# Kernel optimization log

Hardware: AMD Instinct MI355X
Metric: run time of the kernel (lower is better)

The kernel has to match this reference:

```python
import jax, jax.numpy as jnp
import numpy as np
from jax import lax

PATCH = 17
THRESH = 0.5


def _bbox_from_mask(mask_np):
    # mask_np: [D,H,W] bool. Matches mask_to_3d_bbox (min/max of nonzero coords).
    z, y, x = np.nonzero(mask_np)
    return (int(x.min()), int(y.min()), int(z.min()),
            int(x.max()), int(y.max()), int(z.max()))


def _extract_patches(vol, bbox):
    # vol: [1,1,D,H,W]; crop uses exclusive max (slice z_min:z_max) like the torch code
    x0, y0, z0, x1, y1, z1 = bbox
    t = vol[:, :, z0:z1, y0:y1, x0:x1]
    pads = []
    for d in t.shape[2:]:
        r = d % PATCH
        p = (PATCH - r) % PATCH
        pads.append((p // 2, p - p // 2))
    t = jnp.pad(t, ((0, 0), (0, 0), pads[0], pads[1], pads[2]))
    D, H, W = t.shape[2:]
    nD, nH, nW = D // PATCH, H // PATCH, W // PATCH
    p = t.reshape(nD, PATCH, nH, PATCH, nW, PATCH)
    p = p.transpose(0, 2, 4, 1, 3, 5).reshape(-1, PATCH, PATCH, PATCH)
    return p[:, None]  # [N,1,17,17,17]


def _conv3d(x, w, b, stride):
    y = lax.conv_general_dilated(x, w, (stride,) * 3, 'VALID',
                                 dimension_numbers=('NCDHW', 'OIDHW', 'NCDHW'))
    return y + b.reshape(1, -1, 1, 1, 1)


def _model(fixed, moving, c1w, c1b, c2w, c2b, f1w, f1b, f2w, f2b):
    # Stand-in for the opaque torch.jit model: siamese-concat 3D CNN -> MLP -> tanh.
    x = jnp.concatenate([fixed, moving], axis=1)          # [N,2,17,17,17]
    x = jax.nn.relu(_conv3d(x, c1w, c1b, 2))              # [N,32,8,8,8]
    x = jax.nn.relu(_conv3d(x, c2w, c2b, 2))              # [N,64,3,3,3]
    x = x.reshape(x.shape[0], -1)                         # [N,1728]
    x = jax.nn.relu(x @ f1w.T + f1b)                      # [N,256]
    return jnp.tanh(x @ f2w.T + f2b)                      # [N,1]


def setup_inputs() -> dict:
    key = jax.random.key(0)
    ks = jax.random.split(key, 10)
    V = 222
    source = jax.random.normal(ks[0], (1, 1, V, V, V), jnp.float32)
    target = jax.random.uniform(ks[1], (1, 1, V, V, V), jnp.float32)
    fc_in = 64 * 3 * 3 * 3
    return {
        'source': source,
        'target': target,
        'conv1_w': jax.random.normal(ks[2], (32, 2, 3, 3, 3), jnp.float32) * 0.1,
        'conv1_b': jnp.zeros((32,), jnp.float32),
        'conv2_w': jax.random.normal(ks[3], (64, 32, 3, 3, 3), jnp.float32) * 0.05,
        'conv2_b': jnp.zeros((64,), jnp.float32),
        'fc1_w': jax.random.normal(ks[4], (256, fc_in), jnp.float32) * 0.02,
        'fc1_b': jnp.zeros((256,), jnp.float32),
        'fc2_w': jax.random.normal(ks[5], (1, 256), jnp.float32) * 0.05,
        'fc2_b': jnp.zeros((1,), jnp.float32),
    }


def reference(source, target, conv1_w, conv1_b, conv2_w, conv2_b,
              fc1_w, fc1_b, fc2_w, fc2_b):
    mask_np = np.asarray(target) > 0
    bbox = _bbox_from_mask(mask_np.squeeze())
    fixed_patches = _extract_patches(target, bbox)   # [N,1,17,17,17]
    moving_patches = _extract_patches(source, bbox)
    # per-patch zero fraction on fixed patches; keep if <= threshold
    zero_frac = jnp.mean((fixed_patches[:, 0] == 0).astype(jnp.float32), axis=(1, 2, 3))
    keep = (zero_frac <= THRESH).astype(jnp.float32)  # [N]
    out = _model(fixed_patches, moving_patches, conv1_w, conv1_b, conv2_w, conv2_b,
                 fc1_w, fc1_b, fc2_w, fc2_b)          # [N,1]
    # mean over kept patches == weighted mean (stream-compaction-free, same math)
    return jnp.sum(out[:, 0] * keep) / jnp.sum(keep)
```

## Files before the change

kernel.cpp:

```cpp
#include <hip/hip_runtime.h>


static constexpr int kPS = 433;
static constexpr int kRS = 25;
static constexpr int kCS = 528;
static constexpr int kZS = 66;
static constexpr int kHOff = 6912;

template <bool PACKED>
static __device__ __forceinline__ float2 dmr16_patch(
    int p, int t,
    const float* __restrict__ src, const float* __restrict__ tgt,
    const float* __restrict__ c1w, const float* __restrict__ c1b,
    const float* __restrict__ c2w, const float* __restrict__ c2b,
    const float* __restrict__ fw,  const float* __restrict__ f1b,
    const float* __restrict__ f2w, const float* __restrict__ f2b,
    float* __restrict__ sBuf, float* __restrict__ sRed) {
  int pd = p / 169; int rem = p - pd * 169; int phh = rem / 13; int pww = rem - phh * 13;
  int z0 = pd * 17, y0 = phh * 17, x0 = pww * 17;

  int wv  = t >> 6;
  int od  = (t >> 3) & 7, oh = t & 7;
  int oc2 = t & 63;

  float cnt = 0.f;
  for (int idx = t; idx < 4913; idx += 256) {
    int a = idx / 289; int r2 = idx - a * 289; int b = r2 / 17; int c = r2 - b * 17;
    float v = tgt[((size_t)(z0 + a) * 222 + (y0 + b)) * 222 + (x0 + c)];
    sBuf[a * kPS + b * kRS + c] = v;
    if (v == 0.0f) cnt += 1.f;
  }
  sRed[t] = cnt;
  __syncthreads();
  for (int o = 128; o > 0; o >>= 1) {
    if (t < o) sRed[t] += sRed[t + o];
    __syncthreads();
  }
  float keep = (sRed[0] / 4913.0f <= 0.5f) ? 1.0f : 0.0f;
  __syncthreads();

  float acc2[27];
  #pragma unroll
  for (int i = 0; i < 27; i++) acc2[i] = 0.f;

  #pragma unroll 1
  for (int half = 0; half < 2; half++) {
    float acc[4][8];
    #pragma unroll
    for (int i = 0; i < 4; i++)
      #pragma unroll
      for (int j = 0; j < 8; j++) acc[i][j] = 0.f;

    #pragma unroll 1
    for (int ic = 0; ic < 2; ic++) {
      if (half + ic > 0) {
        const float* vol = ic ? src : tgt;
        __syncthreads();
        for (int idx = t; idx < 4913; idx += 256) {
          int a = idx / 289; int r2 = idx - a * 289; int b = r2 / 17; int c = r2 - b * 17;
          sBuf[a * kPS + b * kRS + c] =
              vol[((size_t)(z0 + a) * 222 + (y0 + b)) * 222 + (x0 + c)];
        }
        __syncthreads();
      }
      #pragma unroll 1
      for (int td = 0; td < 3; td++) {
        #pragma unroll 1
        for (int th = 0; th < 3; th++) {
          int rbase = (2 * od + td) * kPS + (2 * oh + th) * kRS;
          float a[17];
          #pragma unroll
          for (int x = 0; x < 17; x++) a[x] = sBuf[rbase + x];
          #pragma unroll
          for (int ocr = 0; ocr < 4; ocr++) {
            int oc = half * 16 + wv * 4 + ocr;
            const float* wp = c1w + oc * 54 + ic * 27 + td * 9 + th * 3;
            float w0 = wp[0], w1 = wp[1], w2 = wp[2];
            #pragma unroll
            for (int ow = 0; ow < 8; ow++)
              acc[ocr][ow] += a[2 * ow] * w0 + a[2 * ow + 1] * w1 + a[2 * ow + 2] * w2;
          }
        }
      }
    }
    __syncthreads();
    #pragma unroll
    for (int ocr = 0; ocr < 4; ocr++) {
      int lo = wv * 4 + ocr;
      float b = c1b[half * 16 + lo];
      int base = lo * kCS + od * kZS + oh * 8;
      #pragma unroll
      for (int ow = 0; ow < 8; ow++)
        sBuf[base + ow] = fmaxf(acc[ocr][ow] + b, 0.f);
    }
    __syncthreads();

    #pragma unroll 1
    for (int icr = 0; icr < 4; icr++) {
      int icl = wv * 4 + icr;
      int ic  = half * 16 + icl;
      const float* cbase = sBuf + icl * kCS;
      #pragma unroll 1
      for (int td = 0; td < 3; td++) {
        #pragma unroll 1
        for (int th = 0; th < 3; th++) {
          const float* wp = c2w + oc2 * 864 + ic * 27 + td * 9 + th * 3;
          float w0 = wp[0], w1 = wp[1], w2 = wp[2];
          #pragma unroll
          for (int zo = 0; zo < 3; zo++) {
            #pragma unroll
            for (int yo = 0; yo < 3; yo++) {
              const float* rp = cbase + (2 * zo + td) * kZS + (2 * yo + th) * 8;
              #pragma unroll
              for (int xo = 0; xo < 3; xo++)
                acc2[zo * 9 + yo * 3 + xo] +=
                    rp[2 * xo] * w0 + rp[2 * xo + 1] * w1 + rp[2 * xo + 2] * w2;
            }
          }
        }
      }
    }
  }
  __syncthreads();
  #pragma unroll
  for (int pos = 0; pos < 27; pos++)
    sBuf[(wv * 27 + pos) * 64 + oc2] = acc2[pos];
  __syncthreads();
  float* sH = sBuf + kHOff;
  for (int idx = t; idx < 1728; idx += 256) {
    int o = idx & 63, pos = idx >> 6;
    float v = sBuf[pos * 64 + o] + sBuf[(27 + pos) * 64 + o] +
              sBuf[(54 + pos) * 64 + o] + sBuf[(81 + pos) * 64 + o];
    sH[o * 27 + pos] = fmaxf(v + c2b[o], 0.f);
  }
  __syncthreads();

  float acc1 = 0.f;
  if (PACKED) {
    const float4* w4p = (const float4*)fw;
    const float4* sH4 = (const float4*)sH;
    #pragma unroll 8
    for (int k4 = 0; k4 < 432; k4++) {
      float4 w  = w4p[k4 * 256 + t];
      float4 hv = sH4[k4];
      acc1 += w.x * hv.x + w.y * hv.y + w.z * hv.z + w.w * hv.w;
    }
  } else {
    const float* frow = fw + (size_t)t * 1728;
    #pragma unroll 8
    for (int k = 0; k < 1728; k++) acc1 += sH[k] * frow[k];
  }
  float h = fmaxf(acc1 + f1b[t], 0.f);
  sRed[t] = h * f2w[t];
  __syncthreads();
  for (int o = 128; o > 0; o >>= 1) {
    if (t < o) sRed[t] += sRed[t + o];
    __syncthreads();
  }
  float2 rk;
  rk.x = tanhf(sRed[0] + f2b[0]) * keep;
  rk.y = keep;
  __syncthreads();
  return rk;
}

__global__ void dmr16_tr(const float* __restrict__ f1w, float* __restrict__ w1t4) {
  int k4 = blockIdx.x;
  int n  = threadIdx.x;
  const float* s = f1w + (size_t)n * 1728 + k4 * 4;
  float4 w;
  w.x = s[0]; w.y = s[1]; w.z = s[2]; w.w = s[3];
  ((float4*)w1t4)[k4 * 256 + n] = w;
}

__global__ __launch_bounds__(256, 4)
void DMMRLoss_52621939310662_kernel(
    const float* __restrict__ src, const float* __restrict__ tgt,
    const float* __restrict__ c1w, const float* __restrict__ c1b,
    const float* __restrict__ c2w, const float* __restrict__ c2b,
    const float* __restrict__ w1t4, const float* __restrict__ f1b,
    const float* __restrict__ f2w, const float* __restrict__ f2b,
    float* __restrict__ pr, float* __restrict__ pk) {
  __shared__ float sBuf[8704];
  __shared__ float sRed[256];
  int t = threadIdx.x;
  float2 rk = dmr16_patch<true>(blockIdx.x, t, src, tgt, c1w, c1b, c2w, c2b,
                                w1t4, f1b, f2w, f2b, sBuf, sRed);
  if (t == 0) { pr[blockIdx.x] = rk.x; pk[blockIdx.x] = rk.y; }
}

__global__ __launch_bounds__(256, 4)
void dmr16_hot_raw(const float* __restrict__ src, const float* __restrict__ tgt,
                   const float* __restrict__ c1w, const float* __restrict__ c1b,
                   const float* __restrict__ c2w, const float* __restrict__ c2b,
                   const float* __restrict__ f1w, const float* __restrict__ f1b,
                   const float* __restrict__ f2w, const float* __restrict__ f2b,
                   float* __restrict__ pr, float* __restrict__ pk) {
  __shared__ float sBuf[8704];
  __shared__ float sRed[256];
  int t = threadIdx.x;
  float2 rk = dmr16_patch<false>(blockIdx.x, t, src, tgt, c1w, c1b, c2w, c2b,
                                 f1w, f1b, f2w, f2b, sBuf, sRed);
  if (t == 0) { pr[blockIdx.x] = rk.x; pk[blockIdx.x] = rk.y; }
}

__global__ void dmr16_reduce(const float* __restrict__ pr, const float* __restrict__ pk,
                             float* __restrict__ out) {
  __shared__ float s1[256], s2[256];
  int t = threadIdx.x;
  float a = 0.f, b = 0.f;
  for (int p = t; p < 2197; p += 256) { a += pr[p]; b += pk[p]; }
  s1[t] = a; s2[t] = b;
  __syncthreads();
  for (int o = 128; o > 0; o >>= 1) {
    if (t < o) { s1[t] += s1[t + o]; s2[t] += s2[t + o]; }
    __syncthreads();
  }
  if (t == 0) out[0] = s1[0] / s2[0];
}

__global__ __launch_bounds__(256, 4)
void dmr16_solo(const float* __restrict__ src, const float* __restrict__ tgt,
                const float* __restrict__ c1w, const float* __restrict__ c1b,
                const float* __restrict__ c2w, const float* __restrict__ c2b,
                const float* __restrict__ f1w, const float* __restrict__ f1b,
                const float* __restrict__ f2w, const float* __restrict__ f2b,
                float* __restrict__ out) {
  __shared__ float sBuf[8704];
  __shared__ float sRed[256];
  __shared__ float sAcc[2];
  int t = threadIdx.x;
  if (t == 0) { sAcc[0] = 0.f; sAcc[1] = 0.f; }
  for (int p = 0; p < 2197; p++) {
    __syncthreads();
    float2 rk = dmr16_patch<false>(p, t, src, tgt, c1w, c1b, c2w, c2b,
                                   f1w, f1b, f2w, f2b, sBuf, sRed);
    if (t == 0) { sAcc[0] += rk.x; sAcc[1] += rk.y; }
  }
  __syncthreads();
  if (t == 0) out[0] = sAcc[0] / sAcc[1];
}

extern "C" void kernel_launch(void* const* d_in, const int* in_sizes, int n_in,
                              void* d_out, int out_size, void* d_ws, size_t ws_size,
                              hipStream_t stream) {
  const float* src = (const float*)d_in[0];
  const float* tgt = (const float*)d_in[1];
  const float* c1w = (const float*)d_in[2];
  const float* c1b = (const float*)d_in[3];
  const float* c2w = (const float*)d_in[4];
  const float* c2b = (const float*)d_in[5];
  const float* f1w = (const float*)d_in[6];
  const float* f1b = (const float*)d_in[7];
  const float* f2w = (const float*)d_in[8];
  const float* f2b = (const float*)d_in[9];
  float* out = (float*)d_out;

  const size_t nW1T = 442368;
  const size_t nPK  = 2 * 2197;
  if (d_ws && ws_size >= (nW1T + nPK) * sizeof(float)) {
    float* w1t4 = (float*)d_ws;
    float* pr   = w1t4 + nW1T;
    float* pk   = pr + 2197;
    dmr16_tr<<<432, 256, 0, stream>>>(f1w, w1t4);
    DMMRLoss_52621939310662_kernel<<<2197, 256, 0, stream>>>(
        src, tgt, c1w, c1b, c2w, c2b, w1t4, f1b, f2w, f2b, pr, pk);
    dmr16_reduce<<<1, 256, 0, stream>>>(pr, pk, out);
  } else if (d_ws && ws_size >= nPK * sizeof(float)) {
    float* pr = (float*)d_ws;
    float* pk = pr + 2197;
    dmr16_hot_raw<<<2197, 256, 0, stream>>>(
        src, tgt, c1w, c1b, c2w, c2b, f1w, f1b, f2w, f2b, pr, pk);
    dmr16_reduce<<<1, 256, 0, stream>>>(pr, pk, out);
  } else {
    dmr16_solo<<<1, 256, 0, stream>>>(
        src, tgt, c1w, c1b, c2w, c2b, f1w, f1b, f2w, f2b, out);
  }
}
```

Before: 437.8 us.

## Repack conv2 weights as float4, vectorize conv1 output stores and conv2 LDS reads

```diff
diff --git a/kernel.cpp b/kernel.cpp
--- a/kernel.cpp
+++ b/kernel.cpp
@@ -3,23 +3,24 @@
 
 static constexpr int kPS = 433;
 static constexpr int kRS = 25;
-static constexpr int kCS = 528;
-static constexpr int kZS = 66;
+static constexpr int kCS = 552;
+static constexpr int kZS = 68;
 static constexpr int kHOff = 6912;
 
-template <bool PACKED>
-static __device__ __forceinline__ float2 dmr16_patch(
+template <bool WPACK>
+static __device__ __forceinline__ float2 dmr17_patch(
     int p, int t,
     const float* __restrict__ src, const float* __restrict__ tgt,
     const float* __restrict__ c1w, const float* __restrict__ c1b,
     const float* __restrict__ c2w, const float* __restrict__ c2b,
-    const float* __restrict__ fw,  const float* __restrict__ f1b,
+    const float* __restrict__ w2t4,
+    const float* __restrict__ fw1, const float* __restrict__ f1b,
     const float* __restrict__ f2w, const float* __restrict__ f2b,
     float* __restrict__ sBuf, float* __restrict__ sRed) {
   int pd = p / 169; int rem = p - pd * 169; int phh = rem / 13; int pww = rem - phh * 13;
   int z0 = pd * 17, y0 = phh * 17, x0 = pww * 17;
 
-  int wv  = t >> 6;
+  int wvu = __builtin_amdgcn_readfirstlane(t >> 6);
   int od  = (t >> 3) & 7, oh = t & 7;
   int oc2 = t & 63;
 
@@ -73,7 +74,7 @@
           for (int x = 0; x < 17; x++) a[x] = sBuf[rbase + x];
           #pragma unroll
           for (int ocr = 0; ocr < 4; ocr++) {
-            int oc = half * 16 + wv * 4 + ocr;
+            int oc = half * 16 + wvu * 4 + ocr;
             const float* wp = c1w + oc * 54 + ic * 27 + td * 9 + th * 3;
             float w0 = wp[0], w1 = wp[1], w2 = wp[2];
             #pragma unroll
@@ -86,35 +87,46 @@
     __syncthreads();
     #pragma unroll
     for (int ocr = 0; ocr < 4; ocr++) {
-      int lo = wv * 4 + ocr;
+      int lo = wvu * 4 + ocr;
       float b = c1b[half * 16 + lo];
       int base = lo * kCS + od * kZS + oh * 8;
-      #pragma unroll
-      for (int ow = 0; ow < 8; ow++)
-        sBuf[base + ow] = fmaxf(acc[ocr][ow] + b, 0.f);
+      float4 v0, v1;
+      v0.x = fmaxf(acc[ocr][0] + b, 0.f); v0.y = fmaxf(acc[ocr][1] + b, 0.f);
+      v0.z = fmaxf(acc[ocr][2] + b, 0.f); v0.w = fmaxf(acc[ocr][3] + b, 0.f);
+      v1.x = fmaxf(acc[ocr][4] + b, 0.f); v1.y = fmaxf(acc[ocr][5] + b, 0.f);
+      v1.z = fmaxf(acc[ocr][6] + b, 0.f); v1.w = fmaxf(acc[ocr][7] + b, 0.f);
+      *(float4*)&sBuf[base]     = v0;
+      *(float4*)&sBuf[base + 4] = v1;
     }
     __syncthreads();
 
     #pragma unroll 1
     for (int icr = 0; icr < 4; icr++) {
-      int icl = wv * 4 + icr;
+      int icl = wvu * 4 + icr;
       int ic  = half * 16 + icl;
       const float* cbase = sBuf + icl * kCS;
       #pragma unroll 1
       for (int td = 0; td < 3; td++) {
-        #pragma unroll 1
+        #pragma unroll
         for (int th = 0; th < 3; th++) {
-          const float* wp = c2w + oc2 * 864 + ic * 27 + td * 9 + th * 3;
-          float w0 = wp[0], w1 = wp[1], w2 = wp[2];
+          float wx, wy, wz;
+          if (WPACK) {
+            float4 w = ((const float4*)w2t4)[((ic * 9 + td * 3 + th) << 6) + oc2];
+            wx = w.x; wy = w.y; wz = w.z;
+          } else {
+            const float* wp = c2w + oc2 * 864 + ic * 27 + td * 9 + th * 3;
+            wx = wp[0]; wy = wp[1]; wz = wp[2];
+          }
           #pragma unroll
           for (int zo = 0; zo < 3; zo++) {
             #pragma unroll
             for (int yo = 0; yo < 3; yo++) {
-              const float* rp = cbase + (2 * zo + td) * kZS + (2 * yo + th) * 8;
-              #pragma unroll
-              for (int xo = 0; xo < 3; xo++)
-                acc2[zo * 9 + yo * 3 + xo] +=
-                    rp[2 * xo] * w0 + rp[2 * xo + 1] * w1 + rp[2 * xo + 2] * w2;
+              const float4* rp4 =
+                  (const float4*)(cbase + (2 * zo + td) * kZS + (2 * yo + th) * 8);
+              float4 r0 = rp4[0], r1 = rp4[1];
+              acc2[zo * 9 + yo * 3 + 0] += r0.x * wx + r0.y * wy + r0.z * wz;
+              acc2[zo * 9 + yo * 3 + 1] += r0.z * wx + r0.w * wy + r1.x * wz;
+              acc2[zo * 9 + yo * 3 + 2] += r1.x * wx + r1.y * wy + r1.z * wz;
             }
           }
         }
@@ -124,7 +136,7 @@
   __syncthreads();
   #pragma unroll
   for (int pos = 0; pos < 27; pos++)
-    sBuf[(wv * 27 + pos) * 64 + oc2] = acc2[pos];
+    sBuf[(wvu * 27 + pos) * 64 + oc2] = acc2[pos];
   __syncthreads();
   float* sH = sBuf + kHOff;
   for (int idx = t; idx < 1728; idx += 256) {
@@ -136,8 +148,8 @@
   __syncthreads();
 
   float acc1 = 0.f;
-  if (PACKED) {
-    const float4* w4p = (const float4*)fw;
+  if (WPACK) {
+    const float4* w4p = (const float4*)fw1;
     const float4* sH4 = (const float4*)sH;
     #pragma unroll 8
     for (int k4 = 0; k4 < 432; k4++) {
@@ -146,7 +158,7 @@
       acc1 += w.x * hv.x + w.y * hv.y + w.z * hv.z + w.w * hv.w;
     }
   } else {
-    const float* frow = fw + (size_t)t * 1728;
+    const float* frow = fw1 + (size_t)t * 1728;
     #pragma unroll 8
     for (int k = 0; k < 1728; k++) acc1 += sH[k] * frow[k];
   }
@@ -164,13 +176,20 @@
   return rk;
 }
 
-__global__ void dmr16_tr(const float* __restrict__ f1w, float* __restrict__ w1t4) {
+__global__ void dmr17_tr(const float* __restrict__ f1w, float* __restrict__ w1t4) {
   int k4 = blockIdx.x;
   int n  = threadIdx.x;
   const float* s = f1w + (size_t)n * 1728 + k4 * 4;
-  float4 w;
-  w.x = s[0]; w.y = s[1]; w.z = s[2]; w.w = s[3];
+  float4 w; w.x = s[0]; w.y = s[1]; w.z = s[2]; w.w = s[3];
   ((float4*)w1t4)[k4 * 256 + n] = w;
+}
+
+__global__ void dmr17_tw2(const float* __restrict__ c2w, float* __restrict__ w2t4) {
+  int gid = blockIdx.x * 256 + threadIdx.x;
+  int icth = gid >> 6, oc = gid & 63;
+  const float* s = c2w + (size_t)oc * 864 + icth * 3;
+  float4 w; w.x = s[0]; w.y = s[1]; w.z = s[2]; w.w = 0.f;
+  ((float4*)w2t4)[gid] = w;
 }
 
 __global__ __launch_bounds__(256, 4)
@@ -178,33 +197,34 @@
     const float* __restrict__ src, const float* __restrict__ tgt,
     const float* __restrict__ c1w, const float* __restrict__ c1b,
     const float* __restrict__ c2w, const float* __restrict__ c2b,
+    const float* __restrict__ w2t4,
     const float* __restrict__ w1t4, const float* __restrict__ f1b,
     const float* __restrict__ f2w, const float* __restrict__ f2b,
     float* __restrict__ pr, float* __restrict__ pk) {
-  __shared__ float sBuf[8704];
+  __shared__ float sBuf[8832];
   __shared__ float sRed[256];
   int t = threadIdx.x;
-  float2 rk = dmr16_patch<true>(blockIdx.x, t, src, tgt, c1w, c1b, c2w, c2b,
-                                w1t4, f1b, f2w, f2b, sBuf, sRed);
+  float2 rk = dmr17_patch<true>(blockIdx.x, t, src, tgt, c1w, c1b, c2w, c2b,
+                                w2t4, w1t4, f1b, f2w, f2b, sBuf, sRed);
   if (t == 0) { pr[blockIdx.x] = rk.x; pk[blockIdx.x] = rk.y; }
 }
 
 __global__ __launch_bounds__(256, 4)
-void dmr16_hot_raw(const float* __restrict__ src, const float* __restrict__ tgt,
+void dmr17_hot_raw(const float* __restrict__ src, const float* __restrict__ tgt,
                    const float* __restrict__ c1w, const float* __restrict__ c1b,
                    const float* __restrict__ c2w, const float* __restrict__ c2b,
                    const float* __restrict__ f1w, const float* __restrict__ f1b,
                    const float* __restrict__ f2w, const float* __restrict__ f2b,
                    float* __restrict__ pr, float* __restrict__ pk) {
-  __shared__ float sBuf[8704];
+  __shared__ float sBuf[8832];
   __shared__ float sRed[256];
   int t = threadIdx.x;
-  float2 rk = dmr16_patch<false>(blockIdx.x, t, src, tgt, c1w, c1b, c2w, c2b,
-                                 f1w, f1b, f2w, f2b, sBuf, sRed);
+  float2 rk = dmr17_patch<false>(blockIdx.x, t, src, tgt, c1w, c1b, c2w, c2b,
+                                 nullptr, f1w, f1b, f2w, f2b, sBuf, sRed);
   if (t == 0) { pr[blockIdx.x] = rk.x; pk[blockIdx.x] = rk.y; }
 }
 
-__global__ void dmr16_reduce(const float* __restrict__ pr, const float* __restrict__ pk,
+__global__ void dmr17_reduce(const float* __restrict__ pr, const float* __restrict__ pk,
                              float* __restrict__ out) {
   __shared__ float s1[256], s2[256];
   int t = threadIdx.x;
@@ -220,21 +240,21 @@
 }
 
 __global__ __launch_bounds__(256, 4)
-void dmr16_solo(const float* __restrict__ src, const float* __restrict__ tgt,
+void dmr17_solo(const float* __restrict__ src, const float* __restrict__ tgt,
                 const float* __restrict__ c1w, const float* __restrict__ c1b,
                 const float* __restrict__ c2w, const float* __restrict__ c2b,
                 const float* __restrict__ f1w, const float* __restrict__ f1b,
                 const float* __restrict__ f2w, const float* __restrict__ f2b,
                 float* __restrict__ out) {
-  __shared__ float sBuf[8704];
+  __shared__ float sBuf[8832];
   __shared__ float sRed[256];
   __shared__ float sAcc[2];
   int t = threadIdx.x;
   if (t == 0) { sAcc[0] = 0.f; sAcc[1] = 0.f; }
   for (int p = 0; p < 2197; p++) {
     __syncthreads();
-    float2 rk = dmr16_patch<false>(p, t, src, tgt, c1w, c1b, c2w, c2b,
-                                   f1w, f1b, f2w, f2b, sBuf, sRed);
+    float2 rk = dmr17_patch<false>(p, t, src, tgt, c1w, c1b, c2w, c2b,
+                                   nullptr, f1w, f1b, f2w, f2b, sBuf, sRed);
     if (t == 0) { sAcc[0] += rk.x; sAcc[1] += rk.y; }
   }
   __syncthreads();
@@ -257,23 +277,26 @@
   float* out = (float*)d_out;
 
   const size_t nW1T = 442368;
+  const size_t nW2T = 73728;
   const size_t nPK  = 2 * 2197;
-  if (d_ws && ws_size >= (nW1T + nPK) * sizeof(float)) {
+  if (d_ws && ws_size >= (nW1T + nW2T + nPK) * sizeof(float)) {
     float* w1t4 = (float*)d_ws;
-    float* pr   = w1t4 + nW1T;
+    float* w2t4 = w1t4 + nW1T;
+    float* pr   = w2t4 + nW2T;
     float* pk   = pr + 2197;
-    dmr16_tr<<<432, 256, 0, stream>>>(f1w, w1t4);
+    dmr17_tr<<<432, 256, 0, stream>>>(f1w, w1t4);
+    dmr17_tw2<<<72, 256, 0, stream>>>(c2w, w2t4);
     DMMRLoss_52621939310662_kernel<<<2197, 256, 0, stream>>>(
-        src, tgt, c1w, c1b, c2w, c2b, w1t4, f1b, f2w, f2b, pr, pk);
-    dmr16_reduce<<<1, 256, 0, stream>>>(pr, pk, out);
+        src, tgt, c1w, c1b, c2w, c2b, w2t4, w1t4, f1b, f2w, f2b, pr, pk);
+    dmr17_reduce<<<1, 256, 0, stream>>>(pr, pk, out);
   } else if (d_ws && ws_size >= nPK * sizeof(float)) {
     float* pr = (float*)d_ws;
     float* pk = pr + 2197;
-    dmr16_hot_raw<<<2197, 256, 0, stream>>>(
+    dmr17_hot_raw<<<2197, 256, 0, stream>>>(
         src, tgt, c1w, c1b, c2w, c2b, f1w, f1b, f2w, f2b, pr, pk);
-    dmr16_reduce<<<1, 256, 0, stream>>>(pr, pk, out);
+    dmr17_reduce<<<1, 256, 0, stream>>>(pr, pk, out);
   } else {
-    dmr16_solo<<<1, 256, 0, stream>>>(
+    dmr17_solo<<<1, 256, 0, stream>>>(
         src, tgt, c1w, c1b, c2w, c2b, f1w, f1b, f2w, f2b, out);
   }
 }
```

Result: slower. 1.008 ms (+130.2%).

## Compute all conv1 channels in one pass and use wave shuffle reductions

Applied to the files above, without the earlier changes.

```diff
diff --git a/kernel.cpp b/kernel.cpp
--- a/kernel.cpp
+++ b/kernel.cpp
@@ -7,13 +7,13 @@
 static constexpr int kZS = 66;
 static constexpr int kHOff = 6912;
 
-template <bool PACKED>
-static __device__ __forceinline__ float2 dmr16_patch(
+template <bool WPACK>
+static __device__ __forceinline__ float2 dmr19_patch(
     int p, int t,
     const float* __restrict__ src, const float* __restrict__ tgt,
     const float* __restrict__ c1w, const float* __restrict__ c1b,
     const float* __restrict__ c2w, const float* __restrict__ c2b,
-    const float* __restrict__ fw,  const float* __restrict__ f1b,
+    const float* __restrict__ fw1, const float* __restrict__ f1b,
     const float* __restrict__ f2w, const float* __restrict__ f2b,
     float* __restrict__ sBuf, float* __restrict__ sRed) {
   int pd = p / 169; int rem = p - pd * 169; int phh = rem / 13; int pww = rem - phh * 13;
@@ -30,75 +30,75 @@
     sBuf[a * kPS + b * kRS + c] = v;
     if (v == 0.0f) cnt += 1.f;
   }
-  sRed[t] = cnt;
-  __syncthreads();
-  for (int o = 128; o > 0; o >>= 1) {
-    if (t < o) sRed[t] += sRed[t + o];
-    __syncthreads();
-  }
-  float keep = (sRed[0] / 4913.0f <= 0.5f) ? 1.0f : 0.0f;
-  __syncthreads();
-
-  float acc2[27];
-  #pragma unroll
-  for (int i = 0; i < 27; i++) acc2[i] = 0.f;
+  #pragma unroll
+  for (int o = 32; o > 0; o >>= 1) cnt += __shfl_down(cnt, o, 64);
+  if ((t & 63) == 0) sRed[wv] = cnt;
+  __syncthreads();
+  float keep = ((sRed[0] + sRed[1] + sRed[2] + sRed[3]) / 4913.0f <= 0.5f) ? 1.0f : 0.0f;
+
+  float acc[8][8];
+  #pragma unroll
+  for (int i = 0; i < 8; i++)
+    #pragma unroll
+    for (int j = 0; j < 8; j++) acc[i][j] = 0.f;
 
   #pragma unroll 1
-  for (int half = 0; half < 2; half++) {
-    float acc[4][8];
-    #pragma unroll
-    for (int i = 0; i < 4; i++)
-      #pragma unroll
-      for (int j = 0; j < 8; j++) acc[i][j] = 0.f;
-
+  for (int ic = 0; ic < 2; ic++) {
+    if (ic == 1) {
+      __syncthreads();
+      for (int idx = t; idx < 4913; idx += 256) {
+        int a = idx / 289; int r2 = idx - a * 289; int b = r2 / 17; int c = r2 - b * 17;
+        sBuf[a * kPS + b * kRS + c] =
+            src[((size_t)(z0 + a) * 222 + (y0 + b)) * 222 + (x0 + c)];
+      }
+      __syncthreads();
+    }
     #pragma unroll 1
-    for (int ic = 0; ic < 2; ic++) {
-      if (half + ic > 0) {
-        const float* vol = ic ? src : tgt;
-        __syncthreads();
-        for (int idx = t; idx < 4913; idx += 256) {
-          int a = idx / 289; int r2 = idx - a * 289; int b = r2 / 17; int c = r2 - b * 17;
-          sBuf[a * kPS + b * kRS + c] =
-              vol[((size_t)(z0 + a) * 222 + (y0 + b)) * 222 + (x0 + c)];
-        }
-        __syncthreads();
-      }
+    for (int td = 0; td < 3; td++) {
       #pragma unroll 1
-      for (int td = 0; td < 3; td++) {
-        #pragma unroll 1
-        for (int th = 0; th < 3; th++) {
-          int rbase = (2 * od + td) * kPS + (2 * oh + th) * kRS;
-          float a[17];
-          #pragma unroll
-          for (int x = 0; x < 17; x++) a[x] = sBuf[rbase + x];
+      for (int th = 0; th < 3; th++) {
+        int rbase = (2 * od + td) * kPS + (2 * oh + th) * kRS;
+        float a[17];
+        #pragma unroll
+        for (int x = 0; x < 17; x++) a[x] = sBuf[rbase + x];
+        #pragma unroll
+        for (int hh = 0; hh < 2; hh++) {
           #pragma unroll
           for (int ocr = 0; ocr < 4; ocr++) {
-            int oc = half * 16 + wv * 4 + ocr;
+            int oc = hh * 16 + wv * 4 + ocr;
             const float* wp = c1w + oc * 54 + ic * 27 + td * 9 + th * 3;
             float w0 = wp[0], w1 = wp[1], w2 = wp[2];
             #pragma unroll
             for (int ow = 0; ow < 8; ow++)
-              acc[ocr][ow] += a[2 * ow] * w0 + a[2 * ow + 1] * w1 + a[2 * ow + 2] * w2;
+              acc[hh * 4 + ocr][ow] += a[2 * ow] * w0 + a[2 * ow + 1] * w1 + a[2 * ow + 2] * w2;
           }
         }
       }
     }
+  }
+
+  float acc2[27];
+  #pragma unroll
+  for (int i = 0; i < 27; i++) acc2[i] = 0.f;
+
+  #pragma unroll 1
+  for (int hh = 0; hh < 2; hh++) {
     __syncthreads();
     #pragma unroll
     for (int ocr = 0; ocr < 4; ocr++) {
       int lo = wv * 4 + ocr;
-      float b = c1b[half * 16 + lo];
+      float b = c1b[hh * 16 + lo];
       int base = lo * kCS + od * kZS + oh * 8;
       #pragma unroll
       for (int ow = 0; ow < 8; ow++)
-        sBuf[base + ow] = fmaxf(acc[ocr][ow] + b, 0.f);
+        sBuf[base + ow] = fmaxf(acc[hh * 4 + ocr][ow] + b, 0.f);
     }
     __syncthreads();
 
     #pragma unroll 1
     for (int icr = 0; icr < 4; icr++) {
       int icl = wv * 4 + icr;
-      int ic  = half * 16 + icl;
+      int ic  = hh * 16 + icl;
       const float* cbase = sBuf + icl * kCS;
       #pragma unroll 1
       for (int td = 0; td < 3; td++) {
@@ -136,8 +136,8 @@
   __syncthreads();
 
   float acc1 = 0.f;
-  if (PACKED) {
-    const float4* w4p = (const float4*)fw;
+  if (WPACK) {
+    const float4* w4p = (const float4*)fw1;
     const float4* sH4 = (const float4*)sH;
     #pragma unroll 8
     for (int k4 = 0; k4 < 432; k4++) {
@@ -146,30 +146,28 @@
       acc1 += w.x * hv.x + w.y * hv.y + w.z * hv.z + w.w * hv.w;
     }
   } else {
-    const float* frow = fw + (size_t)t * 1728;
+    const float* frow = fw1 + (size_t)t * 1728;
     #pragma unroll 8
     for (int k = 0; k < 1728; k++) acc1 += sH[k] * frow[k];
   }
   float h = fmaxf(acc1 + f1b[t], 0.f);
-  sRed[t] = h * f2w[t];
-  __syncthreads();
-  for (int o = 128; o > 0; o >>= 1) {
-    if (t < o) sRed[t] += sRed[t + o];
-    __syncthreads();
-  }
+  float tl = h * f2w[t];
+  #pragma unroll
+  for (int o = 32; o > 0; o >>= 1) tl += __shfl_down(tl, o, 64);
+  if ((t & 63) == 0) sRed[wv] = tl;
+  __syncthreads();
   float2 rk;
-  rk.x = tanhf(sRed[0] + f2b[0]) * keep;
+  rk.x = tanhf(sRed[0] + sRed[1] + sRed[2] + sRed[3] + f2b[0]) * keep;
   rk.y = keep;
   __syncthreads();
   return rk;
 }
 
-__global__ void dmr16_tr(const float* __restrict__ f1w, float* __restrict__ w1t4) {
+__global__ void dmr19_tr(const float* __restrict__ f1w, float* __restrict__ w1t4) {
   int k4 = blockIdx.x;
   int n  = threadIdx.x;
   const float* s = f1w + (size_t)n * 1728 + k4 * 4;
-  float4 w;
-  w.x = s[0]; w.y = s[1]; w.z = s[2]; w.w = s[3];
+  float4 w; w.x = s[0]; w.y = s[1]; w.z = s[2]; w.w = s[3];
   ((float4*)w1t4)[k4 * 256 + n] = w;
 }
 
@@ -182,29 +180,29 @@
     const float* __restrict__ f2w, const float* __restrict__ f2b,
     float* __restrict__ pr, float* __restrict__ pk) {
   __shared__ float sBuf[8704];
-  __shared__ float sRed[256];
-  int t = threadIdx.x;
-  float2 rk = dmr16_patch<true>(blockIdx.x, t, src, tgt, c1w, c1b, c2w, c2b,
+  __shared__ float sRed[4];
+  int t = threadIdx.x;
+  float2 rk = dmr19_patch<true>(blockIdx.x, t, src, tgt, c1w, c1b, c2w, c2b,
                                 w1t4, f1b, f2w, f2b, sBuf, sRed);
   if (t == 0) { pr[blockIdx.x] = rk.x; pk[blockIdx.x] = rk.y; }
 }
 
 __global__ __launch_bounds__(256, 4)
-void dmr16_hot_raw(const float* __restrict__ src, const float* __restrict__ tgt,
+void dmr19_hot_raw(const float* __restrict__ src, const float* __restrict__ tgt,
                    const float* __restrict__ c1w, const float* __restrict__ c1b,
                    const float* __restrict__ c2w, const float* __restrict__ c2b,
                    const float* __restrict__ f1w, const float* __restrict__ f1b,
                    const float* __restrict__ f2w, const float* __restrict__ f2b,
                    float* __restrict__ pr, float* __restrict__ pk) {
   __shared__ float sBuf[8704];
-  __shared__ float sRed[256];
-  int t = threadIdx.x;
-  float2 rk = dmr16_patch<false>(blockIdx.x, t, src, tgt, c1w, c1b, c2w, c2b,
+  __shared__ float sRed[4];
+  int t = threadIdx.x;
+  float2 rk = dmr19_patch<false>(blockIdx.x, t, src, tgt, c1w, c1b, c2w, c2b,
                                  f1w, f1b, f2w, f2b, sBuf, sRed);
   if (t == 0) { pr[blockIdx.x] = rk.x; pk[blockIdx.x] = rk.y; }
 }
 
-__global__ void dmr16_reduce(const float* __restrict__ pr, const float* __restrict__ pk,
+__global__ void dmr19_reduce(const float* __restrict__ pr, const float* __restrict__ pk,
                              float* __restrict__ out) {
   __shared__ float s1[256], s2[256];
   int t = threadIdx.x;
@@ -220,20 +218,20 @@
 }
 
 __global__ __launch_bounds__(256, 4)
-void dmr16_solo(const float* __restrict__ src, const float* __restrict__ tgt,
+void dmr19_solo(const float* __restrict__ src, const float* __restrict__ tgt,
                 const float* __restrict__ c1w, const float* __restrict__ c1b,
                 const float* __restrict__ c2w, const float* __restrict__ c2b,
                 const float* __restrict__ f1w, const float* __restrict__ f1b,
                 const float* __restrict__ f2w, const float* __restrict__ f2b,
                 float* __restrict__ out) {
   __shared__ float sBuf[8704];
-  __shared__ float sRed[256];
+  __shared__ float sRed[4];
   __shared__ float sAcc[2];
   int t = threadIdx.x;
   if (t == 0) { sAcc[0] = 0.f; sAcc[1] = 0.f; }
   for (int p = 0; p < 2197; p++) {
     __syncthreads();
-    float2 rk = dmr16_patch<false>(p, t, src, tgt, c1w, c1b, c2w, c2b,
+    float2 rk = dmr19_patch<false>(p, t, src, tgt, c1w, c1b, c2w, c2b,
                                    f1w, f1b, f2w, f2b, sBuf, sRed);
     if (t == 0) { sAcc[0] += rk.x; sAcc[1] += rk.y; }
   }
@@ -262,18 +260,18 @@
     float* w1t4 = (float*)d_ws;
     float* pr   = w1t4 + nW1T;
     float* pk   = pr + 2197;
-    dmr16_tr<<<432, 256, 0, stream>>>(f1w, w1t4);
+    dmr19_tr<<<432, 256, 0, stream>>>(f1w, w1t4);
     DMMRLoss_52621939310662_kernel<<<2197, 256, 0, stream>>>(
         src, tgt, c1w, c1b, c2w, c2b, w1t4, f1b, f2w, f2b, pr, pk);
-    dmr16_reduce<<<1, 256, 0, stream>>>(pr, pk, out);
+    dmr19_reduce<<<1, 256, 0, stream>>>(pr, pk, out);
   } else if (d_ws && ws_size >= nPK * sizeof(float)) {
     float* pr = (float*)d_ws;
     float* pk = pr + 2197;
-    dmr16_hot_raw<<<2197, 256, 0, stream>>>(
+    dmr19_hot_raw<<<2197, 256, 0, stream>>>(
         src, tgt, c1w, c1b, c2w, c2b, f1w, f1b, f2w, f2b, pr, pk);
-    dmr16_reduce<<<1, 256, 0, stream>>>(pr, pk, out);
+    dmr19_reduce<<<1, 256, 0, stream>>>(pr, pk, out);
   } else {
-    dmr16_solo<<<1, 256, 0, stream>>>(
+    dmr19_solo<<<1, 256, 0, stream>>>(
         src, tgt, c1w, c1b, c2w, c2b, f1w, f1b, f2w, f2b, out);
   }
 }
```

Result: slower. 496.6 us (+13.4%).

## Restructure conv2 loop to reuse LDS rows and vectorize conv1 stores

Applied to the files above, without the earlier changes.

```diff
diff --git a/kernel.cpp b/kernel.cpp
--- a/kernel.cpp
+++ b/kernel.cpp
@@ -3,17 +3,17 @@
 
 static constexpr int kPS = 433;
 static constexpr int kRS = 25;
-static constexpr int kCS = 528;
-static constexpr int kZS = 66;
+static constexpr int kCS = 552;
+static constexpr int kZS = 68;
 static constexpr int kHOff = 6912;
 
-template <bool PACKED>
-static __device__ __forceinline__ float2 dmr16_patch(
+template <bool WPACK>
+static __device__ __forceinline__ float2 dmr21_patch(
     int p, int t,
     const float* __restrict__ src, const float* __restrict__ tgt,
     const float* __restrict__ c1w, const float* __restrict__ c1b,
     const float* __restrict__ c2w, const float* __restrict__ c2b,
-    const float* __restrict__ fw,  const float* __restrict__ f1b,
+    const float* __restrict__ fw1, const float* __restrict__ f1b,
     const float* __restrict__ f2w, const float* __restrict__ f2b,
     float* __restrict__ sBuf, float* __restrict__ sRed) {
   int pd = p / 169; int rem = p - pd * 169; int phh = rem / 13; int pww = rem - phh * 13;
@@ -89,9 +89,13 @@
       int lo = wv * 4 + ocr;
       float b = c1b[half * 16 + lo];
       int base = lo * kCS + od * kZS + oh * 8;
-      #pragma unroll
-      for (int ow = 0; ow < 8; ow++)
-        sBuf[base + ow] = fmaxf(acc[ocr][ow] + b, 0.f);
+      float4 v0, v1;
+      v0.x = fmaxf(acc[ocr][0] + b, 0.f); v0.y = fmaxf(acc[ocr][1] + b, 0.f);
+      v0.z = fmaxf(acc[ocr][2] + b, 0.f); v0.w = fmaxf(acc[ocr][3] + b, 0.f);
+      v1.x = fmaxf(acc[ocr][4] + b, 0.f); v1.y = fmaxf(acc[ocr][5] + b, 0.f);
+      v1.z = fmaxf(acc[ocr][6] + b, 0.f); v1.w = fmaxf(acc[ocr][7] + b, 0.f);
+      *(float4*)&sBuf[base]     = v0;
+      *(float4*)&sBuf[base + 4] = v1;
     }
     __syncthreads();
 
@@ -100,21 +104,36 @@
       int icl = wv * 4 + icr;
       int ic  = half * 16 + icl;
       const float* cbase = sBuf + icl * kCS;
-      #pragma unroll 1
-      for (int td = 0; td < 3; td++) {
-        #pragma unroll 1
-        for (int th = 0; th < 3; th++) {
-          const float* wp = c2w + oc2 * 864 + ic * 27 + td * 9 + th * 3;
-          float w0 = wp[0], w1 = wp[1], w2 = wp[2];
+      float w[27];
+      {
+        const float* wp = c2w + (size_t)oc2 * 864 + ic * 27;
+        #pragma unroll
+        for (int j = 0; j < 27; j++) w[j] = wp[j];
+      }
+      #pragma unroll
+      for (int zrow = 0; zrow < 7; zrow++) {
+        #pragma unroll
+        for (int yrow = 0; yrow < 7; yrow++) {
+          const float4* rp4 = (const float4*)(cbase + zrow * kZS + yrow * 8);
+          float4 r0 = rp4[0], r1 = rp4[1];
+          float row[8] = {r0.x, r0.y, r0.z, r0.w, r1.x, r1.y, r1.z, r1.w};
           #pragma unroll
-          for (int zo = 0; zo < 3; zo++) {
+          for (int td = 0; td < 3; td++) {
+            int zo2 = zrow - td;
+            if (zo2 < 0 || zo2 > 4 || (zo2 & 1)) continue;
+            int zo = zo2 >> 1;
             #pragma unroll
-            for (int yo = 0; yo < 3; yo++) {
-              const float* rp = cbase + (2 * zo + td) * kZS + (2 * yo + th) * 8;
+            for (int th = 0; th < 3; th++) {
+              int yo2 = yrow - th;
+              if (yo2 < 0 || yo2 > 4 || (yo2 & 1)) continue;
+              int yo = yo2 >> 1;
+              float w0 = w[td * 9 + th * 3 + 0];
+              float w1 = w[td * 9 + th * 3 + 1];
+              float w2 = w[td * 9 + th * 3 + 2];
               #pragma unroll
               for (int xo = 0; xo < 3; xo++)
                 acc2[zo * 9 + yo * 3 + xo] +=
-                    rp[2 * xo] * w0 + rp[2 * xo + 1] * w1 + rp[2 * xo + 2] * w2;
+                    row[2 * xo] * w0 + row[2 * xo + 1] * w1 + row[2 * xo + 2] * w2;
             }
           }
         }
@@ -136,8 +155,8 @@
   __syncthreads();
 
   float acc1 = 0.f;
-  if (PACKED) {
-    const float4* w4p = (const float4*)fw;
+  if (WPACK) {
+    const float4* w4p = (const float4*)fw1;
     const float4* sH4 = (const float4*)sH;
     #pragma unroll 8
     for (int k4 = 0; k4 < 432; k4++) {
@@ -146,7 +165,7 @@
       acc1 += w.x * hv.x + w.y * hv.y + w.z * hv.z + w.w * hv.w;
     }
   } else {
-    const float* frow = fw + (size_t)t * 1728;
+    const float* frow = fw1 + (size_t)t * 1728;
     #pragma unroll 8
     for (int k = 0; k < 1728; k++) acc1 += sH[k] * frow[k];
   }
@@ -164,16 +183,15 @@
   return rk;
 }
 
-__global__ void dmr16_tr(const float* __restrict__ f1w, float* __restrict__ w1t4) {
+__global__ void dmr21_tr(const float* __restrict__ f1w, float* __restrict__ w1t4) {
   int k4 = blockIdx.x;
   int n  = threadIdx.x;
   const float* s = f1w + (size_t)n * 1728 + k4 * 4;
-  float4 w;
-  w.x = s[0]; w.y = s[1]; w.z = s[2]; w.w = s[3];
+  float4 w; w.x = s[0]; w.y = s[1]; w.z = s[2]; w.w = s[3];
   ((float4*)w1t4)[k4 * 256 + n] = w;
 }
 
-__global__ __launch_bounds__(256, 4)
+__global__ __launch_bounds__(256, 2)
 void DMMRLoss_52621939310662_kernel(
     const float* __restrict__ src, const float* __restrict__ tgt,
     const float* __restrict__ c1w, const float* __restrict__ c1b,
@@ -181,30 +199,30 @@
     const float* __restrict__ w1t4, const float* __restrict__ f1b,
     const float* __restrict__ f2w, const float* __restrict__ f2b,
     float* __restrict__ pr, float* __restrict__ pk) {
-  __shared__ float sBuf[8704];
+  __shared__ float sBuf[8832];
   __shared__ float sRed[256];
   int t = threadIdx.x;
-  float2 rk = dmr16_patch<true>(blockIdx.x, t, src, tgt, c1w, c1b, c2w, c2b,
+  float2 rk = dmr21_patch<true>(blockIdx.x, t, src, tgt, c1w, c1b, c2w, c2b,
                                 w1t4, f1b, f2w, f2b, sBuf, sRed);
   if (t == 0) { pr[blockIdx.x] = rk.x; pk[blockIdx.x] = rk.y; }
 }
 
-__global__ __launch_bounds__(256, 4)
-void dmr16_hot_raw(const float* __restrict__ src, const float* __restrict__ tgt,
+__global__ __launch_bounds__(256, 2)
+void dmr21_hot_raw(const float* __restrict__ src, const float* __restrict__ tgt,
                    const float* __restrict__ c1w, const float* __restrict__ c1b,
                    const float* __restrict__ c2w, const float* __restrict__ c2b,
                    const float* __restrict__ f1w, const float* __restrict__ f1b,
                    const float* __restrict__ f2w, const float* __restrict__ f2b,
                    float* __restrict__ pr, float* __restrict__ pk) {
-  __shared__ float sBuf[8704];
+  __shared__ float sBuf[8832];
   __shared__ float sRed[256];
   int t = threadIdx.x;
-  float2 rk = dmr16_patch<false>(blockIdx.x, t, src, tgt, c1w, c1b, c2w, c2b,
+  float2 rk = dmr21_patch<false>(blockIdx.x, t, src, tgt, c1w, c1b, c2w, c2b,
                                  f1w, f1b, f2w, f2b, sBuf, sRed);
   if (t == 0) { pr[blockIdx.x] = rk.x; pk[blockIdx.x] = rk.y; }
 }
 
-__global__ void dmr16_reduce(const float* __restrict__ pr, const float* __restrict__ pk,
+__global__ void dmr21_reduce(const float* __restrict__ pr, const float* __restrict__ pk,
                              float* __restrict__ out) {
   __shared__ float s1[256], s2[256];
   int t = threadIdx.x;
@@ -219,21 +237,21 @@
   if (t == 0) out[0] = s1[0] / s2[0];
 }
 
-__global__ __launch_bounds__(256, 4)
-void dmr16_solo(const float* __restrict__ src, const float* __restrict__ tgt,
+__global__ __launch_bounds__(256, 2)
+void dmr21_solo(const float* __restrict__ src, const float* __restrict__ tgt,
                 const float* __restrict__ c1w, const float* __restrict__ c1b,
                 const float* __restrict__ c2w, const float* __restrict__ c2b,
                 const float* __restrict__ f1w, const float* __restrict__ f1b,
                 const float* __restrict__ f2w, const float* __restrict__ f2b,
                 float* __restrict__ out) {
-  __shared__ float sBuf[8704];
+  __shared__ float sBuf[8832];
   __shared__ float sRed[256];
   __shared__ float sAcc[2];
   int t = threadIdx.x;
   if (t == 0) { sAcc[0] = 0.f; sAcc[1] = 0.f; }
   for (int p = 0; p < 2197; p++) {
     __syncthreads();
-    float2 rk = dmr16_patch<false>(p, t, src, tgt, c1w, c1b, c2w, c2b,
+    float2 rk = dmr21_patch<false>(p, t, src, tgt, c1w, c1b, c2w, c2b,
                                    f1w, f1b, f2w, f2b, sBuf, sRed);
     if (t == 0) { sAcc[0] += rk.x; sAcc[1] += rk.y; }
   }
@@ -262,18 +280,18 @@
     float* w1t4 = (float*)d_ws;
     float* pr   = w1t4 + nW1T;
     float* pk   = pr + 2197;
-    dmr16_tr<<<432, 256, 0, stream>>>(f1w, w1t4);
+    dmr21_tr<<<432, 256, 0, stream>>>(f1w, w1t4);
     DMMRLoss_52621939310662_kernel<<<2197, 256, 0, stream>>>(
         src, tgt, c1w, c1b, c2w, c2b, w1t4, f1b, f2w, f2b, pr, pk);
-    dmr16_reduce<<<1, 256, 0, stream>>>(pr, pk, out);
+    dmr21_reduce<<<1, 256, 0, stream>>>(pr, pk, out);
   } else if (d_ws && ws_size >= nPK * sizeof(float)) {
     float* pr = (float*)d_ws;
     float* pk = pr + 2197;
-    dmr16_hot_raw<<<2197, 256, 0, stream>>>(
+    dmr21_hot_raw<<<2197, 256, 0, stream>>>(
         src, tgt, c1w, c1b, c2w, c2b, f1w, f1b, f2w, f2b, pr, pk);
-    dmr16_reduce<<<1, 256, 0, stream>>>(pr, pk, out);
+    dmr21_reduce<<<1, 256, 0, stream>>>(pr, pk, out);
   } else {
-    dmr16_solo<<<1, 256, 0, stream>>>(
+    dmr21_solo<<<1, 256, 0, stream>>>(
         src, tgt, c1w, c1b, c2w, c2b, f1w, f1b, f2w, f2b, out);
   }
 }
```

New measurement: 930.0 us. 112% more time.
